# Performance work log

Measured on AMD Instinct MI355X. Metric: run time of the kernel, lower is better.

The kernel has to match this reference:

```python
import jax, jax.numpy as jnp
import numpy as np

B, N, D, H = 2, 2048, 1024, 16
DH = D // H


def setup_inputs() -> dict:
    key = jax.random.key(0)
    ks = jax.random.split(key, 5)
    s = 0.02
    return {
        "x": jax.random.normal(ks[0], (B, N, D), dtype=jnp.float32),
        "Wq": jax.random.normal(ks[1], (D, D), dtype=jnp.float32) * s,
        "Wk": jax.random.normal(ks[2], (D, D), dtype=jnp.float32) * s,
        "Wv": jax.random.normal(ks[3], (D, D), dtype=jnp.float32) * s,
        "Wo": jax.random.normal(ks[4], (D, D), dtype=jnp.float32) * s,
        "bo": jnp.zeros((D,), dtype=jnp.float32),
    }


def reference(x, Wq, Wk, Wv, Wo, bo):
    b, n, d = x.shape
    # linear projections (torch Linear: y = x @ W.T), split into heads -> [b,h,n,dh]
    def proj(W):
        return jnp.einsum('bnd,ed->bne', x, W).reshape(b, n, H, DH).transpose(0, 2, 1, 3)
    q, k, v = proj(Wq), proj(Wk), proj(Wv)
    scores = jnp.einsum('bhqd,bhkd->bhqk', q, k)  # [b,h,n,n]
    causal = jnp.triu(jnp.ones((n, n), dtype=bool), k=1)
    scores = jnp.where(causal, -jnp.inf, scores)
    # NOTE: module scales by 1/sqrt(num_key_tokens), not 1/sqrt(d_head)
    w = jax.nn.softmax(scores / jnp.sqrt(jnp.float32(n)), axis=-1)
    ctx = jnp.einsum('bhqk,bhkd->bhqd', w, v)
    ctx = ctx.transpose(0, 2, 1, 3).reshape(b, n, d)
    return jnp.einsum('bnd,ed->bne', ctx, Wo) + bo
```

## Files before the change

### kernel.cpp

```cpp
#include <hip/hip_runtime.h>
#include <hip/hip_bf16.h>

typedef __attribute__((ext_vector_type(8))) short bf16x8;
typedef __attribute__((ext_vector_type(4))) float f32x4;
typedef __attribute__((ext_vector_type(16))) float f32x16;
typedef unsigned short u16;
typedef unsigned int u32;

__device__ __forceinline__ u16 f2bf(float f) {
  union { float f; unsigned int u; } v; v.f = f;
  return (u16)((v.u + 0x7fffu + ((v.u >> 16) & 1u)) >> 16);
}
__device__ __forceinline__ u32 pack_bf2(float f0, float f1) {
  union { float f; unsigned int u; } a, b; a.f = f0; b.f = f1;
  return __builtin_amdgcn_perm(b.u + 0x8000u, a.u + 0x8000u, 0x07060302u);
}

#define GLOAD_LDS16(g, l) __builtin_amdgcn_global_load_lds( \
    (const __attribute__((address_space(1))) void*)(g),     \
    (__attribute__((address_space(3))) void*)(l), 16, 0, 0)

__global__ __launch_bounds__(256) void conv_all(const float* __restrict__ x,
                                                const float* __restrict__ wq, const float* __restrict__ wk,
                                                const float* __restrict__ wv, const float* __restrict__ wo,
                                                u16* __restrict__ xb, u16* __restrict__ qo, u16* __restrict__ ko,
                                                u16* __restrict__ vo, u16* __restrict__ oo) {
  int y = blockIdx.y;
  const float* src; u16* dst;
  if (y < 4) { src = x + (size_t)y * 1048576; dst = xb + (size_t)y * 1048576; }
  else if (y == 4) { src = wq; dst = qo; }
  else if (y == 5) { src = wk; dst = ko; }
  else if (y == 6) { src = wv; dst = vo; }
  else { src = wo; dst = oo; }
  int i = (blockIdx.x * 256 + threadIdx.x) * 4;
  float4 v = *(const float4*)(src + i);
  ushort4 o;
  o.x = f2bf(v.x); o.y = f2bf(v.y); o.z = f2bf(v.z); o.w = f2bf(v.w);
  *(ushort4*)(dst + i) = o;
}

template <bool SW>
__device__ __forceinline__ void gemm_main(const u16* __restrict__ A, const u16* __restrict__ W,
                                          u16* As, u16* Bs, int m0, int n0, int K,
                                          f32x4 acc[4][4]) {
  int tid = threadIdx.x, wave = tid >> 6, lane = tid & 63;
  int lane15 = lane & 15, quad = lane >> 4;
  int wm = (wave >> 1) * 64, wn = (wave & 1) * 64;
  for (int k0 = 0; k0 < K; k0 += 64) {
    __syncthreads();
#pragma unroll
    for (int i = 0; i < 4; i++) {
      int rbase = wave * 32 + i * 8;
      int rloc = rbase + (lane >> 3);
      int ca = ((lane & 7) ^ (rloc & 7)) * 8;
      GLOAD_LDS16(A + (size_t)(m0 + rloc) * K + k0 + ca, As + rbase * 64);
      GLOAD_LDS16(W + (size_t)(n0 + rloc) * K + k0 + ca, Bs + rbase * 64);
    }
    __syncthreads();
#pragma unroll
    for (int kc = 0; kc < 2; kc++) {
      bf16x8 a[4], b[4];
#pragma unroll
      for (int mi = 0; mi < 4; mi++) {
        int m = wm + mi * 16 + lane15;
        a[mi] = *(const bf16x8*)(As + m * 64 + (((kc * 4 + quad) ^ (m & 7)) * 8));
      }
#pragma unroll
      for (int ni = 0; ni < 4; ni++) {
        int n = wn + ni * 16 + lane15;
        b[ni] = *(const bf16x8*)(Bs + n * 64 + (((kc * 4 + quad) ^ (n & 7)) * 8));
      }
#pragma unroll
      for (int mi = 0; mi < 4; mi++)
#pragma unroll
        for (int ni = 0; ni < 4; ni++)
          acc[mi][ni] = SW ? __builtin_amdgcn_mfma_f32_16x16x32_bf16(b[ni], a[mi], acc[mi][ni], 0, 0, 0)
                           : __builtin_amdgcn_mfma_f32_16x16x32_bf16(a[mi], b[ni], acc[mi][ni], 0, 0, 0);
    }
  }
}

__global__ __launch_bounds__(256, 3) void gemm_qkv(const u16* __restrict__ xb,
                                                   const u16* __restrict__ wq, const u16* __restrict__ wk,
                                                   const u16* __restrict__ wv,
                                                   u16* __restrict__ Qb, u16* __restrict__ Kb,
                                                   u16* __restrict__ Vtg) {
  __shared__ __align__(16) u16 As[128 * 64];
  __shared__ __align__(16) u16 Bs[128 * 64];
  const int K = 1024;
  int z = blockIdx.z;
  const u16* W = (z == 0) ? wq : (z == 1) ? wk : wv;
  int m0 = blockIdx.x * 128, n0 = blockIdx.y * 128;
  f32x4 acc[4][4];
#pragma unroll
  for (int i = 0; i < 4; i++)
#pragma unroll
    for (int j = 0; j < 4; j++) acc[i][j] = (f32x4){0.f, 0.f, 0.f, 0.f};

  int tid = threadIdx.x, wave = tid >> 6, lane = tid & 63;
  int lane15 = lane & 15, quad = lane >> 4;
  int wm = (wave >> 1) * 64, wn = (wave & 1) * 64;
  const float kQs = 0.022097086912079608f * 1.4426950408889634f;

  if (z < 2) {
    gemm_main<true>(xb, W, As, Bs, m0, n0, K, acc);
    u16* Out = z ? Kb : Qb;
    float sc = z ? 1.0f : kQs;
#pragma unroll
    for (int mi = 0; mi < 4; mi++)
#pragma unroll
      for (int ni = 0; ni < 4; ni++) {
        int token = m0 + wm + mi * 16 + lane15;
        int fb = n0 + wn + ni * 16 + quad * 4;
        ushort4 o;
        o.x = f2bf(acc[mi][ni][0] * sc); o.y = f2bf(acc[mi][ni][1] * sc);
        o.z = f2bf(acc[mi][ni][2] * sc); o.w = f2bf(acc[mi][ni][3] * sc);
        *(ushort4*)&Out[(size_t)token * 1024 + fb] = o;
      }
  } else {
    gemm_main<false>(xb, W, As, Bs, m0, n0, K, acc);
#pragma unroll
    for (int mi = 0; mi < 4; mi++)
#pragma unroll
      for (int ni = 0; ni < 4; ni++) {
        int row = m0 + wm + mi * 16 + quad * 4;
        int col = n0 + wn + ni * 16 + lane15;
        int bb = row >> 11, nn = row & 2047;
        ushort4 o;
        o.x = f2bf(acc[mi][ni][0]); o.y = f2bf(acc[mi][ni][1]);
        o.z = f2bf(acc[mi][ni][2]); o.w = f2bf(acc[mi][ni][3]);
        *(ushort4*)&Vtg[(size_t)(bb * 1024 + col) * 2048 + nn] = o;
      }
  }
}

__global__ __launch_bounds__(256, 3) void gemm_out(const u16* __restrict__ A, const u16* __restrict__ W,
                                                   float* __restrict__ Of, const float* __restrict__ bias) {
  __shared__ __align__(16) u16 As[128 * 64];
  __shared__ __align__(16) u16 Bs[128 * 64];
  const int K = 1024;
  int m0 = blockIdx.x * 128, n0 = blockIdx.y * 128;
  f32x4 acc[4][4];
#pragma unroll
  for (int i = 0; i < 4; i++)
#pragma unroll
    for (int j = 0; j < 4; j++) acc[i][j] = (f32x4){0.f, 0.f, 0.f, 0.f};

  gemm_main<true>(A, W, As, Bs, m0, n0, K, acc);

  int tid = threadIdx.x, wave = tid >> 6, lane = tid & 63;
  int lane15 = lane & 15, quad = lane >> 4;
  int wm = (wave >> 1) * 64, wn = (wave & 1) * 64;
#pragma unroll
  for (int mi = 0; mi < 4; mi++)
#pragma unroll
    for (int ni = 0; ni < 4; ni++) {
      int token = m0 + wm + mi * 16 + lane15;
      int fb = n0 + wn + ni * 16 + quad * 4;
      float4 bb = *(const float4*)&bias[fb];
      float4 o;
      o.x = acc[mi][ni][0] + bb.x; o.y = acc[mi][ni][1] + bb.y;
      o.z = acc[mi][ni][2] + bb.z; o.w = acc[mi][ni][3] + bb.w;
      *(float4*)&Of[(size_t)token * 1024 + fb] = o;
    }
}

__global__ __launch_bounds__(256, 4) void attn7(const u16* __restrict__ Q, const u16* __restrict__ Kg,
                                                const u16* __restrict__ Vtg, u16* __restrict__ ctx) {
  __shared__ __align__(16) u16 SH[16384];
  int tid = threadIdx.x, wave = tid >> 6, lane = tid & 63;
  int l31 = lane & 31, hf = lane >> 5;
  int qt = wave & 1, kvh = wave >> 1;

  int bh = blockIdx.x, by = blockIdx.y;
  int sidx = (by < 16) ? (31 - by) : (by - 16);
  int b = bh >> 4, h = bh & 15;
  int qbase = sidx * 64;

  bf16x8 qb[4];
#pragma unroll
  for (int s = 0; s < 4; s++)
    qb[s] = *(const bf16x8*)&Q[(size_t)(b * 2048 + qbase + qt * 32 + l31) * 1024 +
                               h * 64 + s * 16 + hf * 8];

  f32x16 oacc[2];
#pragma unroll
  for (int dt = 0; dt < 2; dt++)
#pragma unroll
    for (int r = 0; r < 16; r++) oacc[dt][r] = 0.f;
  float lsum = 0.f;

  auto stage = [&](int t, int d) {
    int tb = t * 64;
    u16* Kd = SH + d * 4096;
    u16* Vd = SH + 8192 + d * 4096;
#pragma unroll
    for (int i = 0; i < 2; i++) {
      int rbase = wave * 16 + i * 8;
      int rk = rbase + (lane >> 3);
      int ca = ((lane & 7) ^ (rk & 7)) * 8;
      GLOAD_LDS16(&Kg[(size_t)(b * 2048 + tb + rk) * 1024 + h * 64 + ca], Kd + rbase * 64);
      GLOAD_LDS16(&Vtg[(size_t)(b * 1024 + h * 64 + rk) * 2048 + tb + ca], Vd + rbase * 64);
    }
  };

  stage(0, 0);
  for (int t = 0; t <= sidx; ++t) {
    __syncthreads();
    if (t < sidx) stage(t + 1, (t + 1) & 1);
    int d = t & 1;
    const u16* Kd = SH + d * 4096;
    const u16* Vd = SH + 8192 + d * 4096;

    bool diag = (t == sidx);
    if (diag && kvh > qt) continue;

    int krow = kvh * 32 + l31;
    const u16* kp = Kd + krow * 64;
    bf16x8 kf[4];
#pragma unroll
    for (int s = 0; s < 4; s++)
      kf[s] = *(const bf16x8*)(kp + (((2 * s + hf) ^ (krow & 7)) * 8));

    f32x16 sv;
#pragma unroll
    for (int r = 0; r < 16; r++) sv[r] = 0.f;
#pragma unroll
    for (int s = 0; s < 4; s++)
      sv = __builtin_amdgcn_mfma_f32_32x32x16_bf16(kf[s], qb[s], sv, 0, 0, 0);

    if (diag && kvh == qt) {
#pragma unroll
      for (int r = 0; r < 16; r++) {
        int kvloc = (r & 3) + 8 * (r >> 2) + 4 * hf;
        if (kvloc > l31) sv[r] = -10000.0f;
      }
    }
#pragma unroll
    for (int r = 0; r < 16; r++) {
      float p = __builtin_amdgcn_exp2f(sv[r]);
      sv[r] = p; lsum += p;
    }
    u32 p0 = pack_bf2(sv[0], sv[1]),   p1 = pack_bf2(sv[2], sv[3]);
    u32 p2 = pack_bf2(sv[4], sv[5]),   p3 = pack_bf2(sv[6], sv[7]);
    u32 p4 = pack_bf2(sv[8], sv[9]),   p5 = pack_bf2(sv[10], sv[11]);
    u32 p6 = pack_bf2(sv[12], sv[13]), p7 = pack_bf2(sv[14], sv[15]);
    u32 x0 = __shfl_xor(hf ? p0 : p2, 32);
    u32 x1 = __shfl_xor(hf ? p1 : p3, 32);
    u32 x2 = __shfl_xor(hf ? p4 : p6, 32);
    u32 x3 = __shfl_xor(hf ? p5 : p7, 32);
    union U8 { u32 u[4]; bf16x8 v; };
    U8 pf0, pf1;
    pf0.u[0] = hf ? x0 : p0; pf0.u[1] = hf ? x1 : p1;
    pf0.u[2] = hf ? p2 : x0; pf0.u[3] = hf ? p3 : x1;
    pf1.u[0] = hf ? x2 : p4; pf1.u[1] = hf ? x3 : p5;
    pf1.u[2] = hf ? p6 : x2; pf1.u[3] = hf ? p7 : x3;

#pragma unroll
    for (int c = 0; c < 2; c++) {
      bf16x8 pf = c ? pf1.v : pf0.v;
#pragma unroll
      for (int dt = 0; dt < 2; dt++) {
        int vrow = dt * 32 + l31;
        bf16x8 va = *(const bf16x8*)(Vd + vrow * 64 + (((4 * kvh + 2 * c + hf) ^ (vrow & 7)) * 8));
        oacc[dt] = __builtin_amdgcn_mfma_f32_32x32x16_bf16(va, pf, oacc[dt], 0, 0, 0);
      }
    }
  }

  lsum += __shfl_xor(lsum, 32);
  float* MG = (float*)SH;
  float* LS = (float*)(SH + 8192);
  __syncthreads();
  if (kvh == 1) {
#pragma unroll
    for (int dt = 0; dt < 2; dt++) {
      float* p = MG + ((qt * 2 + dt) * 64 + lane) * 16;
#pragma unroll
      for (int gr = 0; gr < 4; gr++)
        *(f32x4*)(p + gr * 4) = (f32x4){oacc[dt][4 * gr], oacc[dt][4 * gr + 1],
                                        oacc[dt][4 * gr + 2], oacc[dt][4 * gr + 3]};
    }
    LS[qt * 32 + l31] = lsum;
  }
  __syncthreads();
  if (kvh == 0) {
    float inv = 1.0f / (lsum + LS[qt * 32 + l31]);
    int token = qbase + qt * 32 + l31;
    size_t off = (size_t)(b * 2048 + token) * 1024 + h * 64;
#pragma unroll
    for (int dt = 0; dt < 2; dt++) {
      const float* p = MG + ((qt * 2 + dt) * 64 + lane) * 16;
#pragma unroll
      for (int gr = 0; gr < 4; gr++) {
        f32x4 m = *(const f32x4*)(p + gr * 4);
        ushort4 o;
        o.x = f2bf((oacc[dt][4 * gr + 0] + m[0]) * inv);
        o.y = f2bf((oacc[dt][4 * gr + 1] + m[1]) * inv);
        o.z = f2bf((oacc[dt][4 * gr + 2] + m[2]) * inv);
        o.w = f2bf((oacc[dt][4 * gr + 3] + m[3]) * inv);
        *(ushort4*)&ctx[off + dt * 32 + 8 * gr + 4 * hf] = o;
      }
    }
  }
}

extern "C" void kernel_launch(void* const* d_in, const int* in_sizes, int n_in,
                              void* d_out, int out_size, void* d_ws, size_t ws_size,
                              hipStream_t stream) {
  const float* x  = (const float*)d_in[0];
  const float* Wq = (const float*)d_in[1];
  const float* Wk = (const float*)d_in[2];
  const float* Wv = (const float*)d_in[3];
  const float* Wo = (const float*)d_in[4];
  const float* bo = (const float*)d_in[5];
  float* out = (float*)d_out;
  char* ws = (char*)d_ws;
  const size_t MB = 1024 * 1024;
  u16* xb   = (u16*)(ws);
  u16* wqb  = (u16*)(ws +  8 * MB);
  u16* wkb  = (u16*)(ws + 10 * MB);
  u16* wvb  = (u16*)(ws + 12 * MB);
  u16* wob  = (u16*)(ws + 14 * MB);
  u16* Qb   = (u16*)(ws + 16 * MB);
  u16* Kb   = (u16*)(ws + 24 * MB);
  u16* Vtg  = (u16*)(ws + 32 * MB);
  u16* ctxb = (u16*)(ws + 40 * MB);

  conv_all<<<dim3(1024, 8), 256, 0, stream>>>(x, Wq, Wk, Wv, Wo, xb, wqb, wkb, wvb, wob);
  gemm_qkv<<<dim3(32, 8, 3), 256, 0, stream>>>(xb, wqb, wkb, wvb, Qb, Kb, Vtg);
  attn7<<<dim3(32, 32), 256, 0, stream>>>(Qb, Kb, Vtg, ctxb);
  gemm_out<<<dim3(32, 8), 256, 0, stream>>>(ctxb, wob, out, bo);
}
```

Baseline: 169.4 us.

## Double-buffer LDS in GEMMs and enlarge QKV tiles to 256x256 with 512 threads

The QKV projection GEMM moves from 128x128 tiles with 256 threads to 256x256 tiles with 8 waves, each wave computing a 128x64 sub-tile. Both GEMMs now double-buffer the LDS tiles, issuing the next K-slice's global-to-LDS loads before the MFMAs on the current slice, with one barrier per iteration instead of two. MFMA sections are wrapped in s_setprio to favour the math waves. The goal is to hide load latency and raise data reuse. The cost is more LDS (128KB per block for QKV), more accumulator registers, and only 192 blocks for QKV, which may underfill the GPU's CUs.

```diff
diff --git a/kernel.cpp b/kernel.cpp
--- a/kernel.cpp
+++ b/kernel.cpp
@@ -40,74 +40,85 @@
 }
 
 template <bool SW>
-__device__ __forceinline__ void gemm_main(const u16* __restrict__ A, const u16* __restrict__ W,
-                                          u16* As, u16* Bs, int m0, int n0, int K,
-                                          f32x4 acc[4][4]) {
+__device__ __forceinline__ void gemm_main256(const u16* __restrict__ A, const u16* __restrict__ W,
+                                             u16 (*As)[16384], u16 (*Bs)[16384],
+                                             int m0, int n0, int K, f32x4 acc[8][4]) {
   int tid = threadIdx.x, wave = tid >> 6, lane = tid & 63;
   int lane15 = lane & 15, quad = lane >> 4;
-  int wm = (wave >> 1) * 64, wn = (wave & 1) * 64;
-  for (int k0 = 0; k0 < K; k0 += 64) {
-    __syncthreads();
-#pragma unroll
-    for (int i = 0; i < 4; i++) {
-      int rbase = wave * 32 + i * 8;
+  int wm = (wave >> 2) * 128, wn = (wave & 3) * 64;
+
+  auto stage = [&](int t, int d) {
+    int k0 = t * 64;
+#pragma unroll
+    for (int s = 0; s < 4; s++) {
+      int rbase = s * 64 + wave * 8;
       int rloc = rbase + (lane >> 3);
       int ca = ((lane & 7) ^ (rloc & 7)) * 8;
-      GLOAD_LDS16(A + (size_t)(m0 + rloc) * K + k0 + ca, As + rbase * 64);
-      GLOAD_LDS16(W + (size_t)(n0 + rloc) * K + k0 + ca, Bs + rbase * 64);
-    }
-    __syncthreads();
+      GLOAD_LDS16(A + (size_t)(m0 + rloc) * K + k0 + ca, As[d] + rbase * 64);
+      GLOAD_LDS16(W + (size_t)(n0 + rloc) * K + k0 + ca, Bs[d] + rbase * 64);
+    }
+  };
+
+  int NT = K / 64;
+  stage(0, 0);
+  __syncthreads();
+  for (int t = 0; t < NT; t++) {
+    int d = t & 1;
+    if (t + 1 < NT) stage(t + 1, d ^ 1);
 #pragma unroll
     for (int kc = 0; kc < 2; kc++) {
-      bf16x8 a[4], b[4];
-#pragma unroll
-      for (int mi = 0; mi < 4; mi++) {
+      bf16x8 a[8], b[4];
+#pragma unroll
+      for (int mi = 0; mi < 8; mi++) {
         int m = wm + mi * 16 + lane15;
-        a[mi] = *(const bf16x8*)(As + m * 64 + (((kc * 4 + quad) ^ (m & 7)) * 8));
+        a[mi] = *(const bf16x8*)(As[d] + m * 64 + (((kc * 4 + quad) ^ (m & 7)) * 8));
       }
 #pragma unroll
       for (int ni = 0; ni < 4; ni++) {
         int n = wn + ni * 16 + lane15;
-        b[ni] = *(const bf16x8*)(Bs + n * 64 + (((kc * 4 + quad) ^ (n & 7)) * 8));
-      }
-#pragma unroll
-      for (int mi = 0; mi < 4; mi++)
+        b[ni] = *(const bf16x8*)(Bs[d] + n * 64 + (((kc * 4 + quad) ^ (n & 7)) * 8));
+      }
+      __builtin_amdgcn_s_setprio(1);
+#pragma unroll
+      for (int mi = 0; mi < 8; mi++)
 #pragma unroll
         for (int ni = 0; ni < 4; ni++)
           acc[mi][ni] = SW ? __builtin_amdgcn_mfma_f32_16x16x32_bf16(b[ni], a[mi], acc[mi][ni], 0, 0, 0)
                            : __builtin_amdgcn_mfma_f32_16x16x32_bf16(a[mi], b[ni], acc[mi][ni], 0, 0, 0);
-    }
-  }
-}
-
-__global__ __launch_bounds__(256, 3) void gemm_qkv(const u16* __restrict__ xb,
+      __builtin_amdgcn_s_setprio(0);
+    }
+    __syncthreads();
+  }
+}
+
+__global__ __launch_bounds__(512, 2) void gemm_qkv(const u16* __restrict__ xb,
                                                    const u16* __restrict__ wq, const u16* __restrict__ wk,
                                                    const u16* __restrict__ wv,
                                                    u16* __restrict__ Qb, u16* __restrict__ Kb,
                                                    u16* __restrict__ Vtg) {
-  __shared__ __align__(16) u16 As[128 * 64];
-  __shared__ __align__(16) u16 Bs[128 * 64];
+  __shared__ __align__(16) u16 As[2][16384];
+  __shared__ __align__(16) u16 Bs[2][16384];
   const int K = 1024;
   int z = blockIdx.z;
   const u16* W = (z == 0) ? wq : (z == 1) ? wk : wv;
-  int m0 = blockIdx.x * 128, n0 = blockIdx.y * 128;
-  f32x4 acc[4][4];
-#pragma unroll
-  for (int i = 0; i < 4; i++)
+  int m0 = blockIdx.x * 256, n0 = blockIdx.y * 256;
+  f32x4 acc[8][4];
+#pragma unroll
+  for (int i = 0; i < 8; i++)
 #pragma unroll
     for (int j = 0; j < 4; j++) acc[i][j] = (f32x4){0.f, 0.f, 0.f, 0.f};
 
   int tid = threadIdx.x, wave = tid >> 6, lane = tid & 63;
   int lane15 = lane & 15, quad = lane >> 4;
-  int wm = (wave >> 1) * 64, wn = (wave & 1) * 64;
+  int wm = (wave >> 2) * 128, wn = (wave & 3) * 64;
   const float kQs = 0.022097086912079608f * 1.4426950408889634f;
 
   if (z < 2) {
-    gemm_main<true>(xb, W, As, Bs, m0, n0, K, acc);
+    gemm_main256<true>(xb, W, As, Bs, m0, n0, K, acc);
     u16* Out = z ? Kb : Qb;
     float sc = z ? 1.0f : kQs;
 #pragma unroll
-    for (int mi = 0; mi < 4; mi++)
+    for (int mi = 0; mi < 8; mi++)
 #pragma unroll
       for (int ni = 0; ni < 4; ni++) {
         int token = m0 + wm + mi * 16 + lane15;
@@ -118,9 +129,9 @@
         *(ushort4*)&Out[(size_t)token * 1024 + fb] = o;
       }
   } else {
-    gemm_main<false>(xb, W, As, Bs, m0, n0, K, acc);
-#pragma unroll
-    for (int mi = 0; mi < 4; mi++)
+    gemm_main256<false>(xb, W, As, Bs, m0, n0, K, acc);
+#pragma unroll
+    for (int mi = 0; mi < 8; mi++)
 #pragma unroll
       for (int ni = 0; ni < 4; ni++) {
         int row = m0 + wm + mi * 16 + quad * 4;
@@ -134,23 +145,62 @@
   }
 }
 
-__global__ __launch_bounds__(256, 3) void gemm_out(const u16* __restrict__ A, const u16* __restrict__ W,
+__global__ __launch_bounds__(256, 2) void gemm_out(const u16* __restrict__ A, const u16* __restrict__ W,
                                                    float* __restrict__ Of, const float* __restrict__ bias) {
-  __shared__ __align__(16) u16 As[128 * 64];
-  __shared__ __align__(16) u16 Bs[128 * 64];
+  __shared__ __align__(16) u16 As[2][8192];
+  __shared__ __align__(16) u16 Bs[2][8192];
   const int K = 1024;
   int m0 = blockIdx.x * 128, n0 = blockIdx.y * 128;
-  f32x4 acc[4][4];
-#pragma unroll
-  for (int i = 0; i < 4; i++)
-#pragma unroll
-    for (int j = 0; j < 4; j++) acc[i][j] = (f32x4){0.f, 0.f, 0.f, 0.f};
-
-  gemm_main<true>(A, W, As, Bs, m0, n0, K, acc);
-
   int tid = threadIdx.x, wave = tid >> 6, lane = tid & 63;
   int lane15 = lane & 15, quad = lane >> 4;
   int wm = (wave >> 1) * 64, wn = (wave & 1) * 64;
+  f32x4 acc[4][4];
+#pragma unroll
+  for (int i = 0; i < 4; i++)
+#pragma unroll
+    for (int j = 0; j < 4; j++) acc[i][j] = (f32x4){0.f, 0.f, 0.f, 0.f};
+
+  auto stage = [&](int t, int d) {
+    int k0 = t * 64;
+#pragma unroll
+    for (int i = 0; i < 4; i++) {
+      int rbase = wave * 32 + i * 8;
+      int rloc = rbase + (lane >> 3);
+      int ca = ((lane & 7) ^ (rloc & 7)) * 8;
+      GLOAD_LDS16(A + (size_t)(m0 + rloc) * K + k0 + ca, As[d] + rbase * 64);
+      GLOAD_LDS16(W + (size_t)(n0 + rloc) * K + k0 + ca, Bs[d] + rbase * 64);
+    }
+  };
+
+  stage(0, 0);
+  __syncthreads();
+  for (int t = 0; t < 16; t++) {
+    int d = t & 1;
+    if (t < 15) stage(t + 1, d ^ 1);
+#pragma unroll
+    for (int kc = 0; kc < 2; kc++) {
+      bf16x8 a[4], b[4];
+#pragma unroll
+      for (int mi = 0; mi < 4; mi++) {
+        int m = wm + mi * 16 + lane15;
+        a[mi] = *(const bf16x8*)(As[d] + m * 64 + (((kc * 4 + quad) ^ (m & 7)) * 8));
+      }
+#pragma unroll
+      for (int ni = 0; ni < 4; ni++) {
+        int n = wn + ni * 16 + lane15;
+        b[ni] = *(const bf16x8*)(Bs[d] + n * 64 + (((kc * 4 + quad) ^ (n & 7)) * 8));
+      }
+      __builtin_amdgcn_s_setprio(1);
+#pragma unroll
+      for (int mi = 0; mi < 4; mi++)
+#pragma unroll
+        for (int ni = 0; ni < 4; ni++)
+          acc[mi][ni] = __builtin_amdgcn_mfma_f32_16x16x32_bf16(b[ni], a[mi], acc[mi][ni], 0, 0, 0);
+      __builtin_amdgcn_s_setprio(0);
+    }
+    __syncthreads();
+  }
+
 #pragma unroll
   for (int mi = 0; mi < 4; mi++)
 #pragma unroll
@@ -328,7 +378,7 @@
   u16* ctxb = (u16*)(ws + 40 * MB);
 
   conv_all<<<dim3(1024, 8), 256, 0, stream>>>(x, Wq, Wk, Wv, Wo, xb, wqb, wkb, wvb, wob);
-  gemm_qkv<<<dim3(32, 8, 3), 256, 0, stream>>>(xb, wqb, wkb, wvb, Qb, Kb, Vtg);
+  gemm_qkv<<<dim3(16, 4, 3), 512, 0, stream>>>(xb, wqb, wkb, wvb, Qb, Kb, Vtg);
   attn7<<<dim3(32, 32), 256, 0, stream>>>(Qb, Kb, Vtg, ctxb);
   gemm_out<<<dim3(32, 8), 256, 0, stream>>>(ctxb, wob, out, bo);
 }
```

Result: slower. 175.1 us (+3.4%).
